# Optimization experiments

Hardware: AMD Instinct MI355X
Metric: run time of the kernel (lower is better)

The kernel has to match this reference:

```python
import jax, jax.numpy as jnp
import numpy as np


def setup_inputs() -> dict:
    key = jax.random.key(0)
    W = jax.random.normal(key, (64, 16, 128, 128), dtype=jnp.float32)
    return {"W": W, "num_iters": 5}


def reference(W, num_iters):
    """Newton-Schulz iterative matrix inverse: X_{k+1} = X_k (2I - W X_k).

    Init: X_0 = W^T / (||W||_1 * ||W||_inf), the classical convergent start.
    W: [..., N, N] batched square matrices.
    """
    n = W.shape[-1]
    absW = jnp.abs(W)
    norm1 = jnp.max(jnp.sum(absW, axis=-2), axis=-1)    # max abs column sum
    norminf = jnp.max(jnp.sum(absW, axis=-1), axis=-1)  # max abs row sum
    scale = (norm1 * norminf)[..., None, None]
    X = jnp.swapaxes(W, -1, -2) / scale
    two_I = 2.0 * jnp.eye(n, dtype=W.dtype)
    for _ in range(num_iters):
        X = jnp.matmul(X, two_I - jnp.matmul(W, X))
    return X
```

## Files before the change

### kernel.cpp

```cpp
#include <hip/hip_runtime.h>


#define NN 128

typedef __attribute__((ext_vector_type(8))) short bf16x8;
typedef __attribute__((ext_vector_type(16))) float f32x16;
typedef __attribute__((ext_vector_type(4))) float f32x4;
typedef __attribute__((ext_vector_type(4))) unsigned short us4;
typedef __attribute__((ext_vector_type(2))) unsigned int u32x2;

#define XRM_OFF   0
#define XCM_OFF   32768
#define SCR_OFF   65536
#define STAGE_OFF 65536
#define RED_OFF   0
#define LDS_BYTES 133120
#define SROW 132

__device__ __forceinline__ unsigned short f2bf(float f) {
  unsigned u = __float_as_uint(f);
  return (unsigned short)((u + 0x7FFFu + ((u >> 16) & 1u)) >> 16);
}
__device__ __forceinline__ float bf2f(unsigned short h) {
  return __uint_as_float(((unsigned)h) << 16);
}
__device__ __forceinline__ f32x16 zero16() {
  f32x16 z;
#pragma unroll
  for (int i = 0; i < 16; ++i) z[i] = 0.0f;
  return z;
}
__device__ __forceinline__ int swz8(int R, int k0) {
  return R * 128 + (((k0 >> 3) ^ (R & 15)) << 3);
}
__device__ __forceinline__ int swz4(int R, int c0) {
  return R * 128 + ((((c0 >> 3) ^ (R & 15)) << 3) | (c0 & 7));
}

__global__ void __launch_bounds__(512)
__attribute__((amdgpu_waves_per_eu(2, 2)))
ns_inverse_kernel(const float* __restrict__ Wglob, const int* __restrict__ nIt,
                  float* __restrict__ outglob) {
  extern __shared__ char lds[];
  unsigned short* xrm = (unsigned short*)(lds + XRM_OFF);
  unsigned short* xcm = (unsigned short*)(lds + XCM_OFF);
  unsigned short* scr = (unsigned short*)(lds + SCR_OFF);
  float* stage = (float*)(lds + STAGE_OFF);
  float* red   = (float*)(lds + RED_OFF);

  const int b = blockIdx.x;
  const float* Wg = Wglob + (size_t)b * (NN * NN);
  float* outg = outglob + (size_t)b * (NN * NN);
  const int t = threadIdx.x;
  const int lane = t & 63;
  const int wv = t >> 6;
  const int l31 = lane & 31;
  const int half = lane >> 5;
  const int s = wv & 3;
  const int g = wv >> 2;
  const int v0 = 2 * g, v1 = 2 * g + 1;
  const int niters = nIt[0];

  {
    const f32x4* src = (const f32x4*)Wg;
#pragma unroll
    for (int i = 0; i < 8; ++i) {
      int idx = t + 512 * i;
      int r = idx >> 5, cp = idx & 31;
      f32x4 val = src[idx];
      *(f32x4*)(stage + r * SROW + 4 * cp) = val;
    }
  }
  __syncthreads();

  if (t < 128) {
    float ssum = 0.f;
    for (int jj = 0; jj < NN; ++jj) { int j = (jj + t) & 127; ssum += fabsf(stage[t * SROW + j]); }
    red[t] = ssum;
  } else if (t < 256) {
    int c = t - 128;
    float ssum = 0.f;
    for (int i = 0; i < NN; ++i) ssum += fabsf(stage[i * SROW + c]);
    red[128 + c] = ssum;
  }
  __syncthreads();
  float mA = fmaxf(red[lane], red[lane + 64]);
  float mB = fmaxf(red[128 + lane], red[192 + lane]);
#pragma unroll
  for (int k = 32; k >= 1; k >>= 1) {
    mA = fmaxf(mA, __shfl_xor(mA, k, 64));
    mB = fmaxf(mB, __shfl_xor(mB, k, 64));
  }
  const float ninf = mA;
  const float n1 = mB;
  const float scale = 1.0f / (n1 * ninf);
  __syncthreads();

  const int pX = 32 * s + l31;
  bf16x8 wfrag[8];
#pragma unroll
  for (int ks = 0; ks < 8; ++ks) {
    const float* src = stage + pX * SROW + 16 * ks + 8 * half;
    f32x4 f0 = *(const f32x4*)(src);
    f32x4 f1 = *(const f32x4*)(src + 4);
    bf16x8 wb;
#pragma unroll
    for (int e = 0; e < 4; ++e) {
      wb[e]     = (short)f2bf(f0[e]);
      wb[4 + e] = (short)f2bf(f1[e]);
    }
    wfrag[ks] = wb;
  }

  {
    const int r = t >> 2;
    const int c0 = (t & 3) * 32;
#pragma unroll
    for (int h = 0; h < 8; ++h) {
      f32x4 a = *(const f32x4*)(stage + r * SROW + c0 + 4 * h);
      us4 hx;
#pragma unroll
      for (int i = 0; i < 4; ++i) hx[i] = f2bf(a[i] * scale);
      *(us4*)(xcm + swz4(r, c0 + 4 * h)) = hx;
    }
  }
  {
    const int r = t & 127;
    const int kc = (t >> 7) * 32;
#pragma unroll
    for (int j4 = 0; j4 < 8; ++j4) {
      int c0 = kc + 4 * j4;
      us4 h4;
#pragma unroll
      for (int i = 0; i < 4; ++i) h4[i] = f2bf(stage[(c0 + i) * SROW + r] * scale);
      *(us4*)(xrm + swz4(r, c0)) = h4;
    }
  }
  __syncthreads();

  const bool oddlane = (lane & 1) != 0;
  const bool swapblk = (lane & 2) != 0;
  const int p0 = 32 * s + (l31 & ~3);
  const int jj = lane & 3;

  const int rv0 = 32 * v0 + l31;
  const int rv1 = 32 * v1 + l31;
  for (int it = 0; it < niters; ++it) {
    const bool last = (it == niters - 1);

#pragma unroll
    for (int i2 = 0; i2 < 2; ++i2) {
      const int rv = i2 ? rv1 : rv0;
      f32x16 tt = zero16();
#pragma unroll
      for (int ks = 0; ks < 8; ++ks) {
        int k0 = ks * 16 + half * 8;
        bf16x8 bv = *(const bf16x8*)(xcm + swz8(rv, k0));
        tt = __builtin_amdgcn_mfma_f32_32x32x16_bf16(wfrag[ks], bv, tt, 0, 0, 0);
      }
#pragma unroll
      for (int q = 0; q < 4; ++q) {
        us4 h4;
#pragma unroll
        for (int i = 0; i < 4; ++i) h4[i] = f2bf(tt[4 * q + i]);
        *(us4*)(scr + swz4(rv, 32 * s + 8 * q + 4 * half)) = h4;
      }
    }
    __syncthreads();

    f32x16 acc0 = zero16(), acc1 = zero16();
#pragma unroll
    for (int ks = 0; ks < 8; ++ks) {
      int k0 = ks * 16 + half * 8;
      bf16x8 bv = *(const bf16x8*)(xrm + swz8(pX, k0));
      bf16x8 a0 = *(const bf16x8*)(scr + swz8(rv0, k0));
      bf16x8 a1 = *(const bf16x8*)(scr + swz8(rv1, k0));
      acc0 = __builtin_amdgcn_mfma_f32_32x32x16_bf16(a0, bv, acc0, 0, 0, 0);
      acc1 = __builtin_amdgcn_mfma_f32_32x32x16_bf16(a1, bv, acc1, 0, 0, 0);
    }
    __syncthreads();

#pragma unroll
    for (int i2 = 0; i2 < 2; ++i2) {
      const int vb = i2 ? v1 : v0;
#pragma unroll
      for (int q = 0; q < 4; ++q) {
        int c0m = 32 * vb + 8 * q + 4 * half;
        int offr = swz4(pX, c0m);
        us4 xh4 = *(const us4*)(xrm + offr);
        f32x4 vv;
#pragma unroll
        for (int i = 0; i < 4; ++i)
          vv[i] = 2.0f * bf2f(xh4[i]) - (i2 ? acc1[4 * q + i] : acc0[4 * q + i]);
        if (last) {
          *(f32x4*)(outg + pX * NN + c0m) = vv;
        } else {
          us4 h4;
#pragma unroll
          for (int i = 0; i < 4; ++i) h4[i] = f2bf(vv[i]);
          *(us4*)(xrm + offr) = h4;
          u32x2 d = __builtin_bit_cast(u32x2, h4);
          unsigned lo = d.x, hi = d.y;
          unsigned p2lo = (unsigned)__builtin_amdgcn_mov_dpp((int)lo, 0x4E, 0xf, 0xf, false);
          unsigned p2hi = (unsigned)__builtin_amdgcn_mov_dpp((int)hi, 0x4E, 0xf, 0xf, false);
          unsigned mlo = swapblk ? p2hi : lo;
          unsigned mhi = swapblk ? hi   : p2lo;
          unsigned p1lo = (unsigned)__builtin_amdgcn_mov_dpp((int)mlo, 0xB1, 0xf, 0xf, false);
          unsigned p1hi = (unsigned)__builtin_amdgcn_mov_dpp((int)mhi, 0xB1, 0xf, 0xf, false);
          u32x2 o;
          unsigned ox_e = (mlo & 0xFFFFu) | (p1lo << 16);
          unsigned ox_o = (p1lo >> 16) | (mlo & 0xFFFF0000u);
          unsigned oy_e = (mhi & 0xFFFFu) | (p1hi << 16);
          unsigned oy_o = (p1hi >> 16) | (mhi & 0xFFFF0000u);
          o.x = oddlane ? ox_o : ox_e;
          o.y = oddlane ? oy_o : oy_e;
          *(u32x2*)(xcm + swz4(c0m + jj, p0)) = o;
        }
      }
    }
    __syncthreads();
  }
}

extern "C" void kernel_launch(void* const* d_in, const int* in_sizes, int n_in,
                              void* d_out, int out_size, void* d_ws, size_t ws_size,
                              hipStream_t stream) {
  const float* W = (const float*)d_in[0];
  const int* nIt = (const int*)d_in[1];
  float* out = (float*)d_out;
  const int nmat = in_sizes[0] / (NN * NN);

  hipFuncSetAttribute((const void*)ns_inverse_kernel,
                      hipFuncAttributeMaxDynamicSharedMemorySize, LDS_BYTES);
  ns_inverse_kernel<<<nmat, 512, LDS_BYTES, stream>>>(W, nIt, out);
}
```

Before: 179.8 us.

## Shrink LDS footprint via chunked staging and in-place scratch to double occupancy

Replaces the full fp32 staging of W with four 32-row chunks using a rotated layout, and has the W*X intermediate overwrite the column-major X buffer in place after its fragments are loaded into registers, with extra barriers. This reduces LDS from about 130KB to 80KB so two blocks can reside per CU, and waves_per_eu is raised to 4 to match. The cost is more barriers in setup and in each iteration, more register pressure from holding 8 B fragments, and a serialized column-sum accumulation.

```diff
diff --git a/kernel.cpp b/kernel.cpp
--- a/kernel.cpp
+++ b/kernel.cpp
@@ -9,13 +9,10 @@
 typedef __attribute__((ext_vector_type(4))) unsigned short us4;
 typedef __attribute__((ext_vector_type(2))) unsigned int u32x2;
 
-#define XRM_OFF   0
-#define XCM_OFF   32768
-#define SCR_OFF   65536
-#define STAGE_OFF 65536
-#define RED_OFF   0
-#define LDS_BYTES 133120
-#define SROW 132
+#define XRM_OFF 0
+#define XCS_OFF 32768
+#define CHK_OFF 65536
+#define LDS_BYTES 81920
 
 __device__ __forceinline__ unsigned short f2bf(float f) {
   unsigned u = __float_as_uint(f);
@@ -36,17 +33,19 @@
 __device__ __forceinline__ int swz4(int R, int c0) {
   return R * 128 + ((((c0 >> 3) ^ (R & 15)) << 3) | (c0 & 7));
 }
+__device__ __forceinline__ int chk_ix(int rr, int c) {
+  return rr * 128 + ((((c >> 2) + rr) & 31) << 2) + (c & 3);
+}
 
 __global__ void __launch_bounds__(512)
-__attribute__((amdgpu_waves_per_eu(2, 2)))
+__attribute__((amdgpu_waves_per_eu(4, 4)))
 ns_inverse_kernel(const float* __restrict__ Wglob, const int* __restrict__ nIt,
                   float* __restrict__ outglob) {
   extern __shared__ char lds[];
   unsigned short* xrm = (unsigned short*)(lds + XRM_OFF);
-  unsigned short* xcm = (unsigned short*)(lds + XCM_OFF);
-  unsigned short* scr = (unsigned short*)(lds + SCR_OFF);
-  float* stage = (float*)(lds + STAGE_OFF);
-  float* red   = (float*)(lds + RED_OFF);
+  unsigned short* xcs = (unsigned short*)(lds + XCS_OFF);
+  float* chk = (float*)(lds + CHK_OFF);
+  float* red = (float*)(lds + XRM_OFF);
 
   const int b = blockIdx.x;
   const float* Wg = Wglob + (size_t)b * (NN * NN);
@@ -61,29 +60,36 @@
   const int v0 = 2 * g, v1 = 2 * g + 1;
   const int niters = nIt[0];
 
-  {
-    const f32x4* src = (const f32x4*)Wg;
-#pragma unroll
-    for (int i = 0; i < 8; ++i) {
+  float colacc = 0.f;
+#pragma unroll
+  for (int c = 0; c < 4; ++c) {
+#pragma unroll
+    for (int i = 0; i < 2; ++i) {
       int idx = t + 512 * i;
-      int r = idx >> 5, cp = idx & 31;
-      f32x4 val = src[idx];
-      *(f32x4*)(stage + r * SROW + 4 * cp) = val;
-    }
-  }
-  __syncthreads();
-
-  if (t < 128) {
-    float ssum = 0.f;
-    for (int jj = 0; jj < NN; ++jj) { int j = (jj + t) & 127; ssum += fabsf(stage[t * SROW + j]); }
-    red[t] = ssum;
-  } else if (t < 256) {
-    int c = t - 128;
-    float ssum = 0.f;
-    for (int i = 0; i < NN; ++i) ssum += fabsf(stage[i * SROW + c]);
-    red[128 + c] = ssum;
-  }
-  __syncthreads();
+      int rr = idx >> 5, c4 = idx & 31;
+      f32x4 v = ((const f32x4*)Wg)[c * 1024 + idx];
+      *(f32x4*)(chk + rr * 128 + (((c4 + rr) & 31) << 2)) = v;
+    }
+    __syncthreads();
+    if (t < 128) {
+      if ((t >> 5) == c) {
+        int rr = t & 31;
+        float ssum = 0.f;
+        for (int jj = 0; jj < 128; ++jj) {
+          int j = (jj + t) & 127;
+          ssum += fabsf(chk[chk_ix(rr, j)]);
+        }
+        red[t] = ssum;
+      }
+    } else if (t < 256) {
+      int cc = t - 128;
+      float sacc = colacc;
+      for (int rr = 0; rr < 32; ++rr) sacc += fabsf(chk[chk_ix(rr, cc)]);
+      colacc = sacc;
+      if (c == 3) red[128 + cc] = sacc;
+    }
+    __syncthreads();
+  }
   float mA = fmaxf(red[lane], red[lane + 64]);
   float mB = fmaxf(red[128 + lane], red[192 + lane]);
 #pragma unroll
@@ -91,52 +97,63 @@
     mA = fmaxf(mA, __shfl_xor(mA, k, 64));
     mB = fmaxf(mB, __shfl_xor(mB, k, 64));
   }
-  const float ninf = mA;
-  const float n1 = mB;
-  const float scale = 1.0f / (n1 * ninf);
-  __syncthreads();
+  const float scale = 1.0f / (mB * mA);
 
   const int pX = 32 * s + l31;
   bf16x8 wfrag[8];
 #pragma unroll
-  for (int ks = 0; ks < 8; ++ks) {
-    const float* src = stage + pX * SROW + 16 * ks + 8 * half;
-    f32x4 f0 = *(const f32x4*)(src);
-    f32x4 f1 = *(const f32x4*)(src + 4);
-    bf16x8 wb;
-#pragma unroll
-    for (int e = 0; e < 4; ++e) {
-      wb[e]     = (short)f2bf(f0[e]);
-      wb[4 + e] = (short)f2bf(f1[e]);
-    }
-    wfrag[ks] = wb;
-  }
-
-  {
-    const int r = t >> 2;
-    const int c0 = (t & 3) * 32;
-#pragma unroll
-    for (int h = 0; h < 8; ++h) {
-      f32x4 a = *(const f32x4*)(stage + r * SROW + c0 + 4 * h);
-      us4 hx;
-#pragma unroll
-      for (int i = 0; i < 4; ++i) hx[i] = f2bf(a[i] * scale);
-      *(us4*)(xcm + swz4(r, c0 + 4 * h)) = hx;
-    }
-  }
-  {
-    const int r = t & 127;
-    const int kc = (t >> 7) * 32;
-#pragma unroll
-    for (int j4 = 0; j4 < 8; ++j4) {
-      int c0 = kc + 4 * j4;
-      us4 h4;
-#pragma unroll
-      for (int i = 0; i < 4; ++i) h4[i] = f2bf(stage[(c0 + i) * SROW + r] * scale);
-      *(us4*)(xrm + swz4(r, c0)) = h4;
-    }
-  }
-  __syncthreads();
+  for (int c = 0; c < 4; ++c) {
+#pragma unroll
+    for (int i = 0; i < 2; ++i) {
+      int idx = t + 512 * i;
+      int rr = idx >> 5, c4 = idx & 31;
+      f32x4 v = ((const f32x4*)Wg)[c * 1024 + idx];
+      *(f32x4*)(chk + rr * 128 + (((c4 + rr) & 31) << 2)) = v;
+    }
+    __syncthreads();
+    {
+      int rr = t >> 4;
+      int r = 32 * c + rr;
+      int c0 = (t & 15) * 8;
+#pragma unroll
+      for (int h = 0; h < 2; ++h) {
+        int cg = (c0 >> 2) + h;
+        f32x4 a = *(const f32x4*)(chk + rr * 128 + (((cg + rr) & 31) << 2));
+        us4 hx;
+#pragma unroll
+        for (int i = 0; i < 4; ++i) hx[i] = f2bf(a[i] * scale);
+        *(us4*)(xcs + swz4(r, c0 + 4 * h)) = hx;
+      }
+    }
+    {
+      int r = t & 127;
+      int rr0 = (t >> 7) * 8;
+      us4 h4a, h4b;
+#pragma unroll
+      for (int k = 0; k < 4; ++k) h4a[k] = f2bf(chk[chk_ix(rr0 + k, r)] * scale);
+#pragma unroll
+      for (int k = 0; k < 4; ++k) h4b[k] = f2bf(chk[chk_ix(rr0 + 4 + k, r)] * scale);
+      *(us4*)(xrm + swz4(r, 32 * c + rr0)) = h4a;
+      *(us4*)(xrm + swz4(r, 32 * c + rr0 + 4)) = h4b;
+    }
+    if (s == c) {
+      int rr = l31;
+#pragma unroll
+      for (int ks = 0; ks < 8; ++ks) {
+        int cg = 4 * ks + 2 * half;
+        f32x4 f0 = *(const f32x4*)(chk + rr * 128 + (((cg + rr) & 31) << 2));
+        f32x4 f1 = *(const f32x4*)(chk + rr * 128 + ((((cg + 1) + rr) & 31) << 2));
+        bf16x8 wb;
+#pragma unroll
+        for (int e = 0; e < 4; ++e) {
+          wb[e] = (short)f2bf(f0[e]);
+          wb[4 + e] = (short)f2bf(f1[e]);
+        }
+        wfrag[ks] = wb;
+      }
+    }
+    __syncthreads();
+  }
 
   const bool oddlane = (lane & 1) != 0;
   const bool swapblk = (lane & 2) != 0;
@@ -148,22 +165,39 @@
   for (int it = 0; it < niters; ++it) {
     const bool last = (it == niters - 1);
 
-#pragma unroll
-    for (int i2 = 0; i2 < 2; ++i2) {
-      const int rv = i2 ? rv1 : rv0;
+    bf16x8 bv[8];
+#pragma unroll
+    for (int ks = 0; ks < 8; ++ks)
+      bv[ks] = *(const bf16x8*)(xcs + swz8(rv0, ks * 16 + half * 8));
+    __syncthreads();
+    {
       f32x16 tt = zero16();
 #pragma unroll
-      for (int ks = 0; ks < 8; ++ks) {
-        int k0 = ks * 16 + half * 8;
-        bf16x8 bv = *(const bf16x8*)(xcm + swz8(rv, k0));
-        tt = __builtin_amdgcn_mfma_f32_32x32x16_bf16(wfrag[ks], bv, tt, 0, 0, 0);
-      }
+      for (int ks = 0; ks < 8; ++ks)
+        tt = __builtin_amdgcn_mfma_f32_32x32x16_bf16(wfrag[ks], bv[ks], tt, 0, 0, 0);
 #pragma unroll
       for (int q = 0; q < 4; ++q) {
         us4 h4;
 #pragma unroll
         for (int i = 0; i < 4; ++i) h4[i] = f2bf(tt[4 * q + i]);
-        *(us4*)(scr + swz4(rv, 32 * s + 8 * q + 4 * half)) = h4;
+        *(us4*)(xcs + swz4(rv0, 32 * s + 8 * q + 4 * half)) = h4;
+      }
+    }
+#pragma unroll
+    for (int ks = 0; ks < 8; ++ks)
+      bv[ks] = *(const bf16x8*)(xcs + swz8(rv1, ks * 16 + half * 8));
+    __syncthreads();
+    {
+      f32x16 tt = zero16();
+#pragma unroll
+      for (int ks = 0; ks < 8; ++ks)
+        tt = __builtin_amdgcn_mfma_f32_32x32x16_bf16(wfrag[ks], bv[ks], tt, 0, 0, 0);
+#pragma unroll
+      for (int q = 0; q < 4; ++q) {
+        us4 h4;
+#pragma unroll
+        for (int i = 0; i < 4; ++i) h4[i] = f2bf(tt[4 * q + i]);
+        *(us4*)(xcs + swz4(rv1, 32 * s + 8 * q + 4 * half)) = h4;
       }
     }
     __syncthreads();
@@ -172,11 +206,11 @@
 #pragma unroll
     for (int ks = 0; ks < 8; ++ks) {
       int k0 = ks * 16 + half * 8;
-      bf16x8 bv = *(const bf16x8*)(xrm + swz8(pX, k0));
-      bf16x8 a0 = *(const bf16x8*)(scr + swz8(rv0, k0));
-      bf16x8 a1 = *(const bf16x8*)(scr + swz8(rv1, k0));
-      acc0 = __builtin_amdgcn_mfma_f32_32x32x16_bf16(a0, bv, acc0, 0, 0, 0);
-      acc1 = __builtin_amdgcn_mfma_f32_32x32x16_bf16(a1, bv, acc1, 0, 0, 0);
+      bf16x8 bvx = *(const bf16x8*)(xrm + swz8(pX, k0));
+      bf16x8 a0 = *(const bf16x8*)(xcs + swz8(rv0, k0));
+      bf16x8 a1 = *(const bf16x8*)(xcs + swz8(rv1, k0));
+      acc0 = __builtin_amdgcn_mfma_f32_32x32x16_bf16(a0, bvx, acc0, 0, 0, 0);
+      acc1 = __builtin_amdgcn_mfma_f32_32x32x16_bf16(a1, bvx, acc1, 0, 0, 0);
     }
     __syncthreads();
 
@@ -214,7 +248,7 @@
           unsigned oy_o = (p1hi >> 16) | (mhi & 0xFFFF0000u);
           o.x = oddlane ? ox_o : ox_e;
           o.y = oddlane ? oy_o : oy_e;
-          *(u32x2*)(xcm + swz4(c0m + jj, p0)) = o;
+          *(u32x2*)(xcs + swz4(c0m + jj, p0)) = o;
         }
       }
     }
```

Measured after the change: 177.6 us. About the same (-1.2%).
